# Performance work log

Measured on AMD Instinct MI355X. Metric: run time of the kernel, lower is better.

## Reference

```python
import jax, jax.numpy as jnp
import numpy as np

DIM = 512
HEADS = 8
DIM_HEAD = 64
NUM_MEM_KV = 4
H = W = 128


def setup_inputs() -> dict:
    key = jax.random.key(0)
    k1, k2, k3, k4 = jax.random.split(key, 4)
    return {
        "x": jax.random.normal(k1, (DIM, H, W), dtype=jnp.float32),
        "norm1_gamma": jnp.zeros((DIM, 1, 1), dtype=jnp.float32),
        "qkv_w": jax.random.normal(k2, (3 * HEADS * DIM_HEAD, DIM), dtype=jnp.float32) * (DIM ** -0.5),
        "mem_kv": jax.random.normal(k3, (2, HEADS, DIM_HEAD, NUM_MEM_KV), dtype=jnp.float32),
        "conv_w": jax.random.normal(k4, (DIM, HEADS * DIM_HEAD), dtype=jnp.float32) * ((HEADS * DIM_HEAD) ** -0.5),
        "conv_b": jnp.zeros((DIM,), dtype=jnp.float32),
        "norm2_gamma": jnp.zeros((DIM, 1, 1), dtype=jnp.float32),
    }


def rms_norm(x, gamma, dim):
    # x: (c, h, w); L2 norm over channel axis, rescale by sqrt(dim)*(gamma+1)
    n = jnp.linalg.norm(x, ord=2, axis=0)  # (h, w)
    return x / n * (gamma + 1.0) * (dim ** 0.5)


def reference(x, norm1_gamma, qkv_w, mem_kv, conv_w, conv_b, norm2_gamma):
    c, h, w = x.shape
    scale = DIM_HEAD ** -0.5
    xn = rms_norm(x, norm1_gamma, DIM)
    # 1x1 conv == channel matmul
    qkv = jnp.einsum('oc,cxy->oxy', qkv_w, xn)  # (3*hidden, h, w)
    q, k, v = jnp.split(qkv, 3, axis=0)
    def to_heads(t):
        return t.reshape(HEADS, DIM_HEAD, h * w)  # (H, d, n)
    q, k, v = to_heads(q), to_heads(k), to_heads(v)
    mk, mv = mem_kv[0], mem_kv[1]  # (H, d, m)
    k = jnp.concatenate([mk, k], axis=-1)
    v = jnp.concatenate([mv, v], axis=-1)
    q = jax.nn.softmax(q, axis=-2) * scale  # softmax over feature dim d
    k = jax.nn.softmax(k, axis=-1)          # softmax over sequence dim n
    context = jnp.einsum('hdn,hen->hde', k, v)  # (H, d, e)
    out = jnp.einsum('hde,hdn->hen', context, q)  # (H, e, n)
    out = out.reshape(HEADS * DIM_HEAD, h, w)
    out = jnp.einsum('oc,cxy->oxy', conv_w, out) + conv_b[:, None, None]
    return rms_norm(out, norm2_gamma, DIM)
```

## Files before the change

### kernel.cpp

```cpp
#include <hip/hip_runtime.h>
#include <hip/hip_bf16.h>
#include <cstdint>


typedef unsigned short u16;
typedef unsigned int   u32;
typedef short bf16x8 __attribute__((ext_vector_type(8)));
typedef float f32x4  __attribute__((ext_vector_type(4)));

#define HW    16384
#define CDIM  512
#define SQRTD 22.627416997969522f

#define WAITV0 asm volatile("s_waitcnt vmcnt(0)" ::: "memory")
#define WAITL0 asm volatile("s_waitcnt lgkmcnt(0)" ::: "memory")
#define SCHED0 __builtin_amdgcn_sched_barrier(0)

__device__ __forceinline__ u16 f2bf(float f) {
  u32 x = __builtin_bit_cast(u32, f);
  u32 r = x + 0x7fffu + ((x >> 16) & 1u);
  return (u16)(r >> 16);
}

__device__ __forceinline__ void gload16(const void* g, void* l) {
  __builtin_amdgcn_global_load_lds(
      (const __attribute__((address_space(1))) void*)(uintptr_t)g,
      (__attribute__((address_space(3))) void*)(u32)(uintptr_t)l,
      16, 0, 0);
}

__global__ __launch_bounds__(512) void k_pre(const float* __restrict__ x, const float* __restrict__ g1,
                                             const float* __restrict__ qkvw, const float* __restrict__ memkv,
                                             u16* __restrict__ xnt, u16* __restrict__ wbf,
                                             float* __restrict__ den, float* __restrict__ ctx16) {
  __shared__ float tl[512 * 68];
  __shared__ float ssp[8][64];
  __shared__ float rs[64];
  __shared__ float gl[512];
  int t = threadIdx.x, l = t & 63, w = t >> 6;
  int b = blockIdx.x;
  int p0 = b * 64;
  #pragma unroll
  for (int i = 0; i < 16; i++) {
    int idx = i * 512 + t;
    int c = idx >> 4, p4 = (idx & 15) * 4;
    float4 v = *(const float4*)(x + (size_t)c * HW + p0 + p4);
    *(float4*)&tl[c * 68 + p4] = v;
  }
  if (t < 512) gl[t] = 1.0f + g1[t];
  {
    float4 z = make_float4(0.f, 0.f, 0.f, 0.f);
    *(float4*)(ctx16 + (size_t)b * 2048 + t * 4) = z;
  }
  __syncthreads();
  {
    float s = 0.f;
    #pragma unroll
    for (int c = 0; c < 64; c++) {
      float v = tl[(w * 64 + c) * 68 + l];
      s += v * v;
    }
    ssp[w][l] = s;
  }
  __syncthreads();
  if (t < 64) {
    float s = 0.f;
    #pragma unroll
    for (int j = 0; j < 8; j++) s += ssp[j][t];
    rs[t] = SQRTD * rsqrtf(s);
  }
  __syncthreads();
  #pragma unroll
  for (int i = 0; i < 8; i++) {
    int c0 = (i * 8 + w) * 8;
    float sp = rs[l];
    u32 pk[4];
    #pragma unroll
    for (int j = 0; j < 4; j++) {
      float a = tl[(c0 + 2 * j) * 68 + l] * sp * gl[c0 + 2 * j];
      float bq = tl[(c0 + 2 * j + 1) * 68 + l] * sp * gl[c0 + 2 * j + 1];
      pk[j] = (u32)f2bf(a) | ((u32)f2bf(bq) << 16);
    }
    *(uint4*)&xnt[(size_t)(p0 + l) * CDIM + c0] = make_uint4(pk[0], pk[1], pk[2], pk[3]);
  }
  #pragma unroll
  for (int sweep = 0; sweep < 2; sweep++) {
    int idx = (sweep * 256 * 512 + b * 512 + t) * 4;
    if (idx < 1536 * 512) {
      float4 v = *(const float4*)(qkvw + idx);
      ushort4 o; o.x = f2bf(v.x); o.y = f2bf(v.y); o.z = f2bf(v.z); o.w = f2bf(v.w);
      *(ushort4*)(wbf + idx) = o;
    }
  }
  if (b == 0 && t < 512) {
    int h = t >> 6, d = t & 63;
    const float* mk = memkv + ((size_t)h * 64 + d) * 4;
    den[t] = __expf(mk[0]) + __expf(mk[1]) + __expf(mk[2]) + __expf(mk[3]);
  }
}

__global__ __launch_bounds__(256, 2) void k_gemm1(const u16* __restrict__ A, const u16* __restrict__ Bt,
                                                  u16* __restrict__ qT, float* __restrict__ den,
                                                  float* __restrict__ ctx16) {
  const int K = CDIM;
  __shared__ u16 As[2][128 * 64], Bs[2][128 * 64];
  __shared__ float dred[2][64];
  int t = threadIdx.x;
  int lane = t & 63, w = t >> 6;
  int lq = lane >> 4, lr = lane & 15;
  int wg = blockIdx.x;
  int gt = (wg & 7) * 192 + (wg >> 3);
  int bn = gt / 12, bm = gt % 12;
  int wm = (w >> 1) * 64, wn = (w & 1) * 64;
  int h = bm - 4;
  int rb01 = (bm < 4) ? bm * 128 : 512 + h * 64;
  int rb23 = (bm < 4) ? bm * 128 : 960 + h * 64;
  f32x4 acc[4][4] = {};
  const u16* Bbase = Bt + (size_t)bn * 128 * K;

  auto STAGE_A = [&](int buf, int kt) {
    #pragma unroll
    for (int i = 0; i < 4; i++) {
      int s = i * 256 + t;
      int row = s >> 3, slot = (s & 7) ^ (row & 7);
      int rb = (i < 2) ? rb01 : rb23;
      gload16(A + (size_t)(rb + row) * K + kt * 64 + slot * 8, &As[buf][(i * 256 + (w << 6)) * 8]);
    }
  };
  auto STAGE_B = [&](int buf, int kt) {
    #pragma unroll
    for (int i = 0; i < 4; i++) {
      int s = i * 256 + t;
      int row = s >> 3, slot = (s & 7) ^ (row & 7);
      gload16(Bbase + (size_t)row * K + kt * 64 + slot * 8, &Bs[buf][(i * 256 + (w << 6)) * 8]);
    }
  };
  auto FRAGS = [&](int buf, int kk, bf16x8* af, bf16x8* bv) {
    #pragma unroll
    for (int mi = 0; mi < 4; mi++) {
      int row = wm + mi * 16 + lr;
      int slot = ((kk << 2) + lq) ^ (row & 7);
      af[mi] = *(const bf16x8*)&As[buf][row * 64 + slot * 8];
    }
    #pragma unroll
    for (int nj = 0; nj < 4; nj++) {
      int row = wn + nj * 16 + lr;
      int slot = ((kk << 2) + lq) ^ (row & 7);
      bv[nj] = *(const bf16x8*)&Bs[buf][row * 64 + slot * 8];
    }
  };

  STAGE_A(0, 0);
  STAGE_B(0, 0);
  WAITV0;
  __builtin_amdgcn_s_barrier();
  SCHED0;
  for (int kt = 0; kt < 8; kt++) {
    int buf = kt & 1;
    bf16x8 af0[4], bv0[4], af1[4], bv1[4];
    FRAGS(buf, 0, af0, bv0);
    if (kt < 7) STAGE_A(buf ^ 1, kt + 1);
    WAITL0;
    SCHED0;
    __builtin_amdgcn_s_setprio(1);
    #pragma unroll
    for (int mi = 0; mi < 4; mi++)
      #pragma unroll
      for (int nj = 0; nj < 4; nj++)
        acc[mi][nj] = __builtin_amdgcn_mfma_f32_16x16x32_bf16(af0[mi], bv0[nj], acc[mi][nj], 0, 0, 0);
    __builtin_amdgcn_s_setprio(0);
    FRAGS(buf, 1, af1, bv1);
    if (kt < 7) STAGE_B(buf ^ 1, kt + 1);
    WAITL0;
    SCHED0;
    __builtin_amdgcn_s_setprio(1);
    #pragma unroll
    for (int mi = 0; mi < 4; mi++)
      #pragma unroll
      for (int nj = 0; nj < 4; nj++)
        acc[mi][nj] = __builtin_amdgcn_mfma_f32_16x16x32_bf16(af1[mi], bv1[nj], acc[mi][nj], 0, 0, 0);
    __builtin_amdgcn_s_setprio(0);
    if (kt < 7) {
      WAITV0;
      __builtin_amdgcn_s_barrier();
      SCHED0;
    }
  }

  if (bm < 4) {
    int cm0 = bm * 128 + wm, cn0 = bn * 128 + wn;
    #pragma unroll
    for (int nj = 0; nj < 4; nj++) {
      float e[4][4];
      float s = 0.f;
      #pragma unroll
      for (int mi = 0; mi < 4; mi++)
        #pragma unroll
        for (int r = 0; r < 4; r++) { e[mi][r] = __expf(acc[mi][nj][r]); s += e[mi][r]; }
      s += __shfl_xor(s, 16);
      s += __shfl_xor(s, 32);
      float inv = 1.0f / s;
      int col = cn0 + nj * 16 + lr;
      #pragma unroll
      for (int mi = 0; mi < 4; mi++) {
        ushort4 o;
        o.x = f2bf(e[mi][0] * inv); o.y = f2bf(e[mi][1] * inv);
        o.z = f2bf(e[mi][2] * inv); o.w = f2bf(e[mi][3] * inv);
        *(ushort4*)&qT[(size_t)col * CDIM + cm0 + mi * 16 + lq * 4] = o;
      }
    }
  } else {
    __syncthreads();
    u16* Ks = &As[0][0];
    u16* Vs = &Bs[0][0];
    if (w < 2) {
      #pragma unroll
      for (int mi = 0; mi < 4; mi++)
        #pragma unroll
        for (int r = 0; r < 4; r++) {
          int d = mi * 16 + lq * 4 + r;
          float rsum = 0.f;
          #pragma unroll
          for (int nj = 0; nj < 4; nj++) {
            float e = __expf(acc[mi][nj][r]);
            rsum += e;
            int px = wn + nj * 16 + lr;
            Ks[d * 128 + (((px >> 3) ^ (d & 7)) << 3) + (px & 7)] = f2bf(e);
          }
          rsum += __shfl_xor(rsum, 1); rsum += __shfl_xor(rsum, 2);
          rsum += __shfl_xor(rsum, 4); rsum += __shfl_xor(rsum, 8);
          if (lr == 0) dred[w][d] = rsum;
        }
    } else {
      #pragma unroll
      for (int mi = 0; mi < 4; mi++)
        #pragma unroll
        for (int r = 0; r < 4; r++) {
          int e = mi * 16 + lq * 4 + r;
          #pragma unroll
          for (int nj = 0; nj < 4; nj++) {
            int px = wn + nj * 16 + lr;
            Vs[e * 128 + (((px >> 3) ^ (e & 7)) << 3) + (px & 7)] = f2bf(acc[mi][nj][r]);
          }
        }
    }
    __syncthreads();
    if (t < 64) atomicAdd(&den[h * 64 + t], dred[0][t] + dred[1][t]);
    f32x4 c2[4] = {};
    #pragma unroll
    for (int ks = 0; ks < 4; ks++) {
      int ra = w * 16 + lr;
      bf16x8 a = *(const bf16x8*)&Ks[ra * 128 + (((ks * 4 + lq) ^ (ra & 7)) << 3)];
      #pragma unroll
      for (int nj = 0; nj < 4; nj++) {
        int rb2 = nj * 16 + lr;
        bf16x8 b = *(const bf16x8*)&Vs[rb2 * 128 + (((ks * 4 + lq) ^ (rb2 & 7)) << 3)];
        c2[nj] = __builtin_amdgcn_mfma_f32_16x16x32_bf16(a, b, c2[nj], 0, 0, 0);
      }
    }
    float* cp = ctx16 + ((size_t)(bn & 15) * 8 + h) * 4096;
    #pragma unroll
    for (int nj = 0; nj < 4; nj++)
      #pragma unroll
      for (int r = 0; r < 4; r++) {
        int d = w * 16 + lq * 4 + r, e = nj * 16 + lr;
        atomicAdd(&cp[d * 64 + e], c2[nj][r]);
      }
  }
}

__global__ __launch_bounds__(256) void k_fold(const float* __restrict__ convw, const float* __restrict__ ctx16,
                                              const float* __restrict__ den, const float* __restrict__ memkv,
                                              u16* __restrict__ Mbf) {
  __shared__ float cn[64 * 65];
  __shared__ float dn[64];
  __shared__ float emk[256];
  __shared__ float smv[256];
  int t = threadIdx.x;
  int h = blockIdx.x & 7, oc = blockIdx.x >> 3;
  if (t < 64) dn[t] = 0.125f / den[h * 64 + t];
  if (t < 256) emk[t] = __expf(memkv[(size_t)h * 256 + t]);
  if (t < 256) smv[t] = memkv[(size_t)(512 * 4) + h * 256 + t];
  __syncthreads();
  #pragma unroll
  for (int i = 0; i < 16; i++) {
    int idx = i * 256 + t;
    int d = idx >> 6, e = idx & 63;
    float s = emk[d * 4] * smv[e * 4] + emk[d * 4 + 1] * smv[e * 4 + 1]
            + emk[d * 4 + 2] * smv[e * 4 + 2] + emk[d * 4 + 3] * smv[e * 4 + 3];
    #pragma unroll
    for (int rep = 0; rep < 16; rep++) s += ctx16[((size_t)rep * 8 + h) * 4096 + idx];
    cn[d * 65 + e] = s * dn[d];
  }
  __syncthreads();
  int o = oc * 64 + (t >> 2);
  int d0 = (t & 3) * 16;
  float Wr[64];
  const float* wp = convw + (size_t)o * CDIM + h * 64;
  #pragma unroll
  for (int e4 = 0; e4 < 16; e4++) {
    float4 v = *(const float4*)(wp + e4 * 4);
    Wr[e4 * 4] = v.x; Wr[e4 * 4 + 1] = v.y; Wr[e4 * 4 + 2] = v.z; Wr[e4 * 4 + 3] = v.w;
  }
  float outv[16];
  #pragma unroll
  for (int dd = 0; dd < 16; dd++) {
    float a = 0.f;
    #pragma unroll
    for (int e = 0; e < 64; e++) a += Wr[e] * cn[(d0 + dd) * 65 + e];
    outv[dd] = a;
  }
  #pragma unroll
  for (int j = 0; j < 8; j++) {
    u32 v = (u32)f2bf(outv[j * 2]) | ((u32)f2bf(outv[j * 2 + 1]) << 16);
    *(u32*)&Mbf[(size_t)o * CDIM + h * 64 + d0 + j * 2] = v;
  }
}

__global__ __launch_bounds__(512) void k_gemm2(const u16* __restrict__ A, const u16* __restrict__ Bt,
                                               const float* __restrict__ bias, const float* __restrict__ g2,
                                               float* __restrict__ out) {
  __shared__ u16 As[512 * 64];
  __shared__ u16 Bs[64 * 64];
  __shared__ float css[64];
  int t = threadIdx.x; int lane = t & 63, w = t >> 6, lq = lane >> 4, lr = lane & 15;
  int bn = blockIdx.x;
  if (t < 64) css[t] = 0.f;
  const u16* Bbase = Bt + (size_t)bn * 64 * CDIM;
  f32x4 acc[4][4] = {};
  for (int kt = 0; kt < 8; kt++) {
    #pragma unroll
    for (int i = 0; i < 8; i++) {
      int s = i * 512 + t;
      int row = s >> 3, slot = (s & 7) ^ (row & 7);
      gload16(A + (size_t)row * CDIM + kt * 64 + slot * 8, &As[(i * 512 + (w << 6)) * 8]);
    }
    {
      int row = t >> 3, slot = (t & 7) ^ (row & 7);
      gload16(Bbase + (size_t)row * CDIM + kt * 64 + slot * 8, &Bs[(w << 6) * 8]);
    }
    __syncthreads();
    #pragma unroll
    for (int kk = 0; kk < 2; kk++) {
      bf16x8 af[4], bv[4];
      #pragma unroll
      for (int mi = 0; mi < 4; mi++) {
        int row = w * 64 + mi * 16 + lr;
        int slot = ((kk << 2) + lq) ^ (row & 7);
        af[mi] = *(const bf16x8*)&As[row * 64 + slot * 8];
      }
      #pragma unroll
      for (int nj = 0; nj < 4; nj++) {
        int row = nj * 16 + lr;
        int slot = ((kk << 2) + lq) ^ (row & 7);
        bv[nj] = *(const bf16x8*)&Bs[row * 64 + slot * 8];
      }
      __builtin_amdgcn_s_setprio(1);
      #pragma unroll
      for (int mi = 0; mi < 4; mi++)
        #pragma unroll
        for (int nj = 0; nj < 4; nj++)
          acc[mi][nj] = __builtin_amdgcn_mfma_f32_16x16x32_bf16(af[mi], bv[nj], acc[mi][nj], 0, 0, 0);
      __builtin_amdgcn_s_setprio(0);
    }
    __syncthreads();
  }
  float bb[4][4];
  float ps[4] = {0.f, 0.f, 0.f, 0.f};
  #pragma unroll
  for (int mi = 0; mi < 4; mi++)
    #pragma unroll
    for (int r = 0; r < 4; r++) {
      int rowg = w * 64 + mi * 16 + lq * 4 + r;
      bb[mi][r] = bias[rowg];
      #pragma unroll
      for (int nj = 0; nj < 4; nj++) {
        float v = acc[mi][nj][r] + bb[mi][r];
        ps[nj] += v * v;
      }
    }
  #pragma unroll
  for (int nj = 0; nj < 4; nj++) {
    ps[nj] += __shfl_xor(ps[nj], 16);
    ps[nj] += __shfl_xor(ps[nj], 32);
  }
  if (lq == 0) {
    #pragma unroll
    for (int nj = 0; nj < 4; nj++) atomicAdd(&css[nj * 16 + lr], ps[nj]);
  }
  __syncthreads();
  float sc[4];
  #pragma unroll
  for (int nj = 0; nj < 4; nj++) sc[nj] = SQRTD * rsqrtf(css[nj * 16 + lr]);
  #pragma unroll
  for (int mi = 0; mi < 4; mi++)
    #pragma unroll
    for (int r = 0; r < 4; r++) {
      int rowg = w * 64 + mi * 16 + lq * 4 + r;
      float g = 1.0f + g2[rowg];
      #pragma unroll
      for (int nj = 0; nj < 4; nj++) {
        float v = acc[mi][nj][r] + bb[mi][r];
        out[(size_t)rowg * HW + bn * 64 + nj * 16 + lr] = v * sc[nj] * g;
      }
    }
}

extern "C" void kernel_launch(void* const* d_in, const int* in_sizes, int n_in,
                              void* d_out, int out_size, void* d_ws, size_t ws_size,
                              hipStream_t stream) {
  (void)in_sizes; (void)n_in; (void)out_size; (void)ws_size;
  const float* x     = (const float*)d_in[0];
  const float* g1    = (const float*)d_in[1];
  const float* qkvw  = (const float*)d_in[2];
  const float* memkv = (const float*)d_in[3];
  const float* convw = (const float*)d_in[4];
  const float* convb = (const float*)d_in[5];
  const float* g2    = (const float*)d_in[6];
  float* out = (float*)d_out;
  char* ws = (char*)d_ws;

  float* den   = (float*)(ws);
  float* ctx16 = (float*)(ws + 4096);
  u16* Mbf     = (u16*)(ws + 2101248);
  u16* wbf     = (u16*)(ws + 2625536);
  u16* xnt     = (u16*)(ws + 4198400);
  u16* qT      = (u16*)(ws + 20975616);

  k_pre<<<256, 512, 0, stream>>>(x, g1, qkvw, memkv, xnt, wbf, den, ctx16);
  k_gemm1<<<1536, 256, 0, stream>>>(wbf, xnt, qT, den, ctx16);
  k_fold<<<64, 256, 0, stream>>>(convw, ctx16, den, memkv, Mbf);
  k_gemm2<<<256, 512, 0, stream>>>(Mbf, qT, convb, g2, out);
}
```

Baseline: 94.98 us.

## Coalesce qT stores via LDS, double-buffer gemm2, split fold across more blocks

The q-softmax epilogue of gemm1 now writes transposed tiles into padded shared memory and then emits 16-byte coalesced global stores, instead of scattered 8-byte stores. The output-projection GEMM gains a two-stage LDS pipeline so the next K tile loads while MFMAs run on the current one. The fold kernel launches twice as many blocks, each computing fewer outputs, to expose more parallelism. The costs are extra barriers and doubled LDS in gemm2, which limits resident blocks per CU.

Result: faster. 91.05 us (-4.1%).

```diff
diff --git a/kernel.cpp b/kernel.cpp
--- a/kernel.cpp
+++ b/kernel.cpp
@@ -188,7 +188,9 @@
   }
 
   if (bm < 4) {
-    int cm0 = bm * 128 + wm, cn0 = bn * 128 + wn;
+    __syncthreads();
+    u16* As0 = &As[0][0];
+    u16* Bs0 = &Bs[0][0];
     #pragma unroll
     for (int nj = 0; nj < 4; nj++) {
       float e[4][4];
@@ -200,13 +202,26 @@
       s += __shfl_xor(s, 16);
       s += __shfl_xor(s, 32);
       float inv = 1.0f / s;
-      int col = cn0 + nj * 16 + lr;
+      int pxl = wn + nj * 16 + lr;
+      u16* lrow = (pxl < 64 ? As0 : Bs0) + (pxl & 63) * 136;
       #pragma unroll
       for (int mi = 0; mi < 4; mi++) {
+        int hdl = wm + mi * 16 + lq * 4;
         ushort4 o;
         o.x = f2bf(e[mi][0] * inv); o.y = f2bf(e[mi][1] * inv);
         o.z = f2bf(e[mi][2] * inv); o.w = f2bf(e[mi][3] * inv);
-        *(ushort4*)&qT[(size_t)col * CDIM + cm0 + mi * 16 + lq * 4] = o;
+        *(ushort4*)&lrow[hdl] = o;
+      }
+    }
+    __syncthreads();
+    {
+      int pxl = t >> 1, half = t & 1;
+      const u16* src = (pxl < 64 ? As0 : Bs0) + (pxl & 63) * 136 + half * 64;
+      u16* dst = &qT[(size_t)(bn * 128 + pxl) * CDIM + bm * 128 + half * 64];
+      #pragma unroll
+      for (int j = 0; j < 8; j++) {
+        uint4 v = *(const uint4*)(src + j * 8);
+        *(uint4*)(dst + j * 8) = v;
       }
     }
   } else {
@@ -293,8 +308,8 @@
     cn[d * 65 + e] = s * dn[d];
   }
   __syncthreads();
-  int o = oc * 64 + (t >> 2);
-  int d0 = (t & 3) * 16;
+  int o = oc * 32 + (t >> 3);
+  int d0 = (t & 7) * 8;
   float Wr[64];
   const float* wp = convw + (size_t)o * CDIM + h * 64;
   #pragma unroll
@@ -302,16 +317,16 @@
     float4 v = *(const float4*)(wp + e4 * 4);
     Wr[e4 * 4] = v.x; Wr[e4 * 4 + 1] = v.y; Wr[e4 * 4 + 2] = v.z; Wr[e4 * 4 + 3] = v.w;
   }
-  float outv[16];
-  #pragma unroll
-  for (int dd = 0; dd < 16; dd++) {
+  float outv[8];
+  #pragma unroll
+  for (int dd = 0; dd < 8; dd++) {
     float a = 0.f;
     #pragma unroll
     for (int e = 0; e < 64; e++) a += Wr[e] * cn[(d0 + dd) * 65 + e];
     outv[dd] = a;
   }
   #pragma unroll
-  for (int j = 0; j < 8; j++) {
+  for (int j = 0; j < 4; j++) {
     u32 v = (u32)f2bf(outv[j * 2]) | ((u32)f2bf(outv[j * 2 + 1]) << 16);
     *(u32*)&Mbf[(size_t)o * CDIM + h * 64 + d0 + j * 2] = v;
   }
@@ -320,51 +335,77 @@
 __global__ __launch_bounds__(512) void k_gemm2(const u16* __restrict__ A, const u16* __restrict__ Bt,
                                                const float* __restrict__ bias, const float* __restrict__ g2,
                                                float* __restrict__ out) {
-  __shared__ u16 As[512 * 64];
-  __shared__ u16 Bs[64 * 64];
+  __shared__ u16 As[2][512 * 64];
+  __shared__ u16 Bs[2][64 * 64];
   __shared__ float css[64];
   int t = threadIdx.x; int lane = t & 63, w = t >> 6, lq = lane >> 4, lr = lane & 15;
   int bn = blockIdx.x;
   if (t < 64) css[t] = 0.f;
   const u16* Bbase = Bt + (size_t)bn * 64 * CDIM;
   f32x4 acc[4][4] = {};
-  for (int kt = 0; kt < 8; kt++) {
+
+  auto STAGE = [&](int buf, int kt) {
     #pragma unroll
     for (int i = 0; i < 8; i++) {
       int s = i * 512 + t;
       int row = s >> 3, slot = (s & 7) ^ (row & 7);
-      gload16(A + (size_t)row * CDIM + kt * 64 + slot * 8, &As[(i * 512 + (w << 6)) * 8]);
+      gload16(A + (size_t)row * CDIM + kt * 64 + slot * 8, &As[buf][(i * 512 + (w << 6)) * 8]);
     }
     {
       int row = t >> 3, slot = (t & 7) ^ (row & 7);
-      gload16(Bbase + (size_t)row * CDIM + kt * 64 + slot * 8, &Bs[(w << 6) * 8]);
-    }
-    __syncthreads();
-    #pragma unroll
-    for (int kk = 0; kk < 2; kk++) {
-      bf16x8 af[4], bv[4];
-      #pragma unroll
-      for (int mi = 0; mi < 4; mi++) {
-        int row = w * 64 + mi * 16 + lr;
-        int slot = ((kk << 2) + lq) ^ (row & 7);
-        af[mi] = *(const bf16x8*)&As[row * 64 + slot * 8];
-      }
-      #pragma unroll
-      for (int nj = 0; nj < 4; nj++) {
-        int row = nj * 16 + lr;
-        int slot = ((kk << 2) + lq) ^ (row & 7);
-        bv[nj] = *(const bf16x8*)&Bs[row * 64 + slot * 8];
-      }
-      __builtin_amdgcn_s_setprio(1);
-      #pragma unroll
-      for (int mi = 0; mi < 4; mi++)
-        #pragma unroll
-        for (int nj = 0; nj < 4; nj++)
-          acc[mi][nj] = __builtin_amdgcn_mfma_f32_16x16x32_bf16(af[mi], bv[nj], acc[mi][nj], 0, 0, 0);
-      __builtin_amdgcn_s_setprio(0);
-    }
-    __syncthreads();
-  }
+      gload16(Bbase + (size_t)row * CDIM + kt * 64 + slot * 8, &Bs[buf][(w << 6) * 8]);
+    }
+  };
+  auto FRAGS = [&](int buf, int kk, bf16x8* af, bf16x8* bv) {
+    #pragma unroll
+    for (int mi = 0; mi < 4; mi++) {
+      int row = w * 64 + mi * 16 + lr;
+      int slot = ((kk << 2) + lq) ^ (row & 7);
+      af[mi] = *(const bf16x8*)&As[buf][row * 64 + slot * 8];
+    }
+    #pragma unroll
+    for (int nj = 0; nj < 4; nj++) {
+      int row = nj * 16 + lr;
+      int slot = ((kk << 2) + lq) ^ (row & 7);
+      bv[nj] = *(const bf16x8*)&Bs[buf][row * 64 + slot * 8];
+    }
+  };
+
+  STAGE(0, 0);
+  WAITV0;
+  __builtin_amdgcn_s_barrier();
+  SCHED0;
+  for (int kt = 0; kt < 8; kt++) {
+    int buf = kt & 1;
+    bf16x8 af0[4], bv0[4], af1[4], bv1[4];
+    FRAGS(buf, 0, af0, bv0);
+    if (kt < 7) STAGE(buf ^ 1, kt + 1);
+    WAITL0;
+    SCHED0;
+    __builtin_amdgcn_s_setprio(1);
+    #pragma unroll
+    for (int mi = 0; mi < 4; mi++)
+      #pragma unroll
+      for (int nj = 0; nj < 4; nj++)
+        acc[mi][nj] = __builtin_amdgcn_mfma_f32_16x16x32_bf16(af0[mi], bv0[nj], acc[mi][nj], 0, 0, 0);
+    __builtin_amdgcn_s_setprio(0);
+    FRAGS(buf, 1, af1, bv1);
+    WAITL0;
+    SCHED0;
+    __builtin_amdgcn_s_setprio(1);
+    #pragma unroll
+    for (int mi = 0; mi < 4; mi++)
+      #pragma unroll
+      for (int nj = 0; nj < 4; nj++)
+        acc[mi][nj] = __builtin_amdgcn_mfma_f32_16x16x32_bf16(af1[mi], bv1[nj], acc[mi][nj], 0, 0, 0);
+    __builtin_amdgcn_s_setprio(0);
+    if (kt < 7) {
+      WAITV0;
+      __builtin_amdgcn_s_barrier();
+      SCHED0;
+    }
+  }
+  __syncthreads();
   float bb[4][4];
   float ps[4] = {0.f, 0.f, 0.f, 0.f};
   #pragma unroll
@@ -429,6 +470,6 @@
 
   k_pre<<<256, 512, 0, stream>>>(x, g1, qkvw, memkv, xnt, wbf, den, ctx16);
   k_gemm1<<<1536, 256, 0, stream>>>(wbf, xnt, qT, den, ctx16);
-  k_fold<<<64, 256, 0, stream>>>(convw, ctx16, den, memkv, Mbf);
+  k_fold<<<128, 256, 0, stream>>>(convw, ctx16, den, memkv, Mbf);
   k_gemm2<<<256, 512, 0, stream>>>(Mbf, qT, convb, g2, out);
 }
```
